# Kernel tuning notes

Measured on AMD Instinct MI355X. Metric: run time of the kernel, lower is better.

The kernel has to match this reference:

```python
import jax, jax.numpy as jnp
import numpy as np

B, T, D_IN, H, L, OUT, S = 128, 256, 8, 512, 2, 2, 32
A = H  # attention_size == hidden_size


def lstm_cell(h, c, xt, Wih, Whh, b):
    # PyTorch LSTM gate order: i, f, g, o ; b = b_ih + b_hh (combined)
    g = xt @ Wih.T + h @ Whh.T + b
    i, f, gg, o = jnp.split(g, 4, axis=-1)
    c = jax.nn.sigmoid(f) * c + jax.nn.sigmoid(i) * jnp.tanh(gg)
    h = jax.nn.sigmoid(o) * jnp.tanh(c)
    return h, c


def setup_inputs() -> dict:
    key = jax.random.key(0)
    ks = jax.random.split(key, 20)
    w = lambda k, shape: jax.random.normal(k, shape, jnp.float32) * 0.1
    return {
        "x": jax.random.normal(ks[0], (B, T, D_IN), jnp.float32),
        # bidirectional encoder, 2 layers; leading dim 2 = (fwd, bwd)
        "enc_Wih0": w(ks[1], (2, 4 * H, D_IN)),
        "enc_Whh0": w(ks[2], (2, 4 * H, H)),
        "enc_b0": w(ks[3], (2, 4 * H)),
        "enc_Wih1": w(ks[4], (2, 4 * H, 2 * H)),
        "enc_Whh1": w(ks[5], (2, 4 * H, H)),
        "enc_b1": w(ks[6], (2, 4 * H)),
        # unidirectional decoder, 2 layers; layer0 input = output_size + 2H
        "dec_Wih0": w(ks[7], (4 * H, 2 * H + OUT)),
        "dec_Whh0": w(ks[8], (4 * H, H)),
        "dec_b0": w(ks[9], (4 * H,)),
        "dec_Wih1": w(ks[10], (4 * H, H)),
        "dec_Whh1": w(ks[11], (4 * H, H)),
        "dec_b1": w(ks[12], (4 * H,)),
        # Bahdanau attention (no biases)
        "Wa": w(ks[13], (A, 2 * H)),
        "Ua": w(ks[14], (A, H)),
        "Va": w(ks[15], (1, A)),
        "proj_W": w(ks[16], (H, H)),
        "proj_b": jnp.zeros((H,), jnp.float32),
        "fc_W": w(ks[17], (OUT, H)),
        "fc_b": jnp.zeros((OUT,), jnp.float32),
    }


def _forward(x, enc_Wih0, enc_Whh0, enc_b0, enc_Wih1, enc_Whh1, enc_b1,
             dec_Wih0, dec_Whh0, dec_b0, dec_Wih1, dec_Whh1, dec_b1,
             Wa, Ua, Va, proj_W, proj_b, fc_W, fc_b):
    Bb = x.shape[0]
    xT = jnp.swapaxes(x, 0, 1)  # [T,B,D]

    def run_dir(seq, Wih, Whh, b, reverse):
        h0 = jnp.zeros((Bb, H), x.dtype)
        def step(carry, xt):
            h, c = lstm_cell(carry[0], carry[1], xt, Wih, Whh, b)
            return (h, c), h
        (hT, cT), hs = jax.lax.scan(step, (h0, h0), seq, reverse=reverse)
        return hs, hT, cT

    # encoder layer 0 (bidirectional)
    of, hf0, cf0 = run_dir(xT, enc_Wih0[0], enc_Whh0[0], enc_b0[0], False)
    ob, hb0, cb0 = run_dir(xT, enc_Wih0[1], enc_Whh0[1], enc_b0[1], True)
    l1in = jnp.concatenate([of, ob], -1)  # [T,B,2H]
    # encoder layer 1
    of1, hf1, cf1 = run_dir(l1in, enc_Wih1[0], enc_Whh1[0], enc_b1[0], False)
    ob1, hb1, cb1 = run_dir(l1in, enc_Wih1[1], enc_Whh1[1], enc_b1[1], True)
    enc_out = jnp.swapaxes(jnp.concatenate([of1, ob1], -1), 0, 1)  # [B,T,2H]

    # torch hidden order: [l0_fwd, l0_bwd, l1_fwd, l1_bwd]; code takes first num_layers=2
    dh = jnp.tanh(jnp.stack([hf0, hb0]) @ proj_W.T + proj_b)  # [2,B,H]
    dc = jnp.stack([cf0, cb0])

    Wa_vals = enc_out @ Wa.T  # [B,T,A], loop-invariant part of attention
    y0 = x[:, -1, :OUT]

    def dec_step(carry, _):
        h, c, y = carry
        q = h[-1]  # [B,H] last-layer hidden
        score = jnp.tanh(Wa_vals + (q @ Ua.T)[:, None, :]) @ Va.T  # [B,T,1]
        wts = jax.nn.softmax(score, axis=1)
        z = jnp.sum(wts * enc_out, axis=1)  # [B,2H]
        h0n, c0n = lstm_cell(h[0], c[0], jnp.concatenate([y, z], 1), dec_Wih0, dec_Whh0, dec_b0)
        h1n, c1n = lstm_cell(h[1], c[1], h0n, dec_Wih1, dec_Whh1, dec_b1)
        yn = h1n @ fc_W.T + fc_b  # [B,OUT]
        return (jnp.stack([h0n, h1n]), jnp.stack([c0n, c1n]), yn), yn

    _, ys = jax.lax.scan(dec_step, (dh, dc, y0), None, length=S)
    return jnp.swapaxes(ys, 0, 1)  # [B,S,OUT]


def reference(x, enc_Wih0, enc_Whh0, enc_b0, enc_Wih1, enc_Whh1, enc_b1,
              dec_Wih0, dec_Whh0, dec_b0, dec_Wih1, dec_Whh1, dec_b1,
              Wa, Ua, Va, proj_W, proj_b, fc_W, fc_b):
    return _forward(x, enc_Wih0, enc_Whh0, enc_b0, enc_Wih1, enc_Whh1, enc_b1,
                    dec_Wih0, dec_Whh0, dec_b0, dec_Wih1, dec_Whh1, dec_b1,
                    Wa, Ua, Va, proj_W, proj_b, fc_W, fc_b)
```

## Files before the change

### kernel.cpp

```cpp
#include <hip/hip_runtime.h>

typedef _Float16 h16;
typedef __attribute__((ext_vector_type(8))) _Float16 f16x8;
typedef __attribute__((ext_vector_type(4))) float f32x4;
typedef unsigned long long u64;
typedef unsigned int u32;
typedef unsigned short u16;

#define B_ 128
#define T_ 256
#define H_ 512
#define S_ 32
#define MFMA __builtin_amdgcn_mfma_f32_16x16x32_f16

#define SLOT_L0F 0
#define SLOT_L0B 257
#define SLOT_ALL 514
#define SLOT_L1F 515
#define SLOT_L1B 771
#define SLOT_DEC 1027

__device__ __forceinline__ float fexp2(float x){ return __builtin_amdgcn_exp2f(x); }
__device__ __forceinline__ float frcp (float x){ return __builtin_amdgcn_rcpf(x); }
__device__ __forceinline__ float fsig (float x){ return frcp(1.f + fexp2(-1.44269504089f*x)); }
__device__ __forceinline__ float ftanh(float x){ return 1.f - 2.f*frcp(1.f + fexp2(2.88539008178f*x)); }

__device__ __forceinline__ f16x8 ld16_coh(const h16* p) {
  u64 q0 = __hip_atomic_load((const u64*)p,     __ATOMIC_RELAXED, __HIP_MEMORY_SCOPE_AGENT);
  u64 q1 = __hip_atomic_load((const u64*)p + 1, __ATOMIC_RELAXED, __HIP_MEMORY_SCOPE_AGENT);
  u64 a[2] = {q0, q1};
  f16x8 v; __builtin_memcpy(&v, a, 16);
  return v;
}
__device__ __forceinline__ float ld4f_coh(const float* p) {
  u32 b = __hip_atomic_load((const u32*)p, __ATOMIC_RELAXED, __HIP_MEMORY_SCOPE_AGENT);
  float v; __builtin_memcpy(&v, &b, 4);
  return v;
}
__device__ __forceinline__ float ld2h_coh(const h16* p) {
  u16 b = __hip_atomic_load((const u16*)p, __ATOMIC_RELAXED, __HIP_MEMORY_SCOPE_AGENT);
  h16 v; __builtin_memcpy(&v, &b, 2);
  return (float)v;
}
__device__ __forceinline__ void st2_coh(h16* p, h16 v) {
  u16 b; __builtin_memcpy(&b, &v, 2);
  __hip_atomic_store((u16*)p, b, __ATOMIC_RELAXED, __HIP_MEMORY_SCOPE_AGENT);
}
__device__ __forceinline__ void st4_coh(float* p, float v) {
  u32 b; __builtin_memcpy(&b, &v, 4);
  __hip_atomic_store((u32*)p, b, __ATOMIC_RELAXED, __HIP_MEMORY_SCOPE_AGENT);
}

__device__ __forceinline__ void bar_arrive(u32* c, int tid) {
  __syncthreads();
  if (tid == 0) atomicAdd(c, 1u);
}
__device__ __forceinline__ void bar_wait(const u32* c, u32 n) {
  while (__hip_atomic_load(c, __ATOMIC_RELAXED, __HIP_MEMORY_SCOPE_AGENT) < n) {}
  __builtin_amdgcn_sched_barrier(0);
}

struct EncP {
  const h16 *xpad, *Wih0, *Whh0, *Wih1, *Whh1;
  const float *b0, *b1;
  h16 *l1in, *encout;
  float *cdump;
  u32* cnt;
};

__global__ __launch_bounds__(512, 1) void encoder_persist(EncP P) {
  const int wg = blockIdx.x, dir = wg >> 7;
  const int j0 = (wg & 127) << 2;
  const int tid = threadIdx.x, wid = tid >> 6, lane = tid & 63;
  const int col = lane & 15, rowg = lane >> 4;
  const int u = col & 3, gt = col >> 2;
  const int m0 = wid << 4;

  __shared__ h16 W[16][1544];

  auto stage = [&](const h16* Wih, int Kx, const h16* Whh) {
    const int CX = Kx >> 3, CT = CX + 64;
    for (int i = tid; i < 16 * CT; i += 512) {
      const int r = i / CT, c = i - r * CT;
      const int grow = (r >> 2) * 512 + j0 + (r & 3);
      f16x8 v = (c < CX) ? *(const f16x8*)(Wih + (size_t)grow * Kx + (c << 3))
                         : *(const f16x8*)(Whh + (size_t)grow * 512 + ((c - CX) << 3));
      *(f16x8*)(&W[r][c << 3]) = v;
    }
  };
  auto pick = [&](float own, float p4, float p8, float p12, int x) {
    return x == 0 ? own : x == 1 ? p4 : x == 2 ? p8 : p12;
  };
  auto xpart0 = [&](int t) -> f32x4 {
    f32x4 a = {0.f, 0.f, 0.f, 0.f};
    f16x8 av = *(const f16x8*)(P.xpad + ((size_t)(m0 + col) * T_ + t) * 32 + rowg * 8);
    f16x8 bv = *(const f16x8*)(&W[col][rowg * 8]);
    return MFMA(av, bv, a, 0, 0, 0);
  };
  auto xpart1 = [&](int t) -> f32x4 {
    f32x4 a = {0.f, 0.f, 0.f, 0.f};
    const h16* ax = P.l1in + ((size_t)t * B_ + m0 + col) * 1024 + rowg * 8;
    #pragma unroll
    for (int ks = 0; ks < 32; ++ks) {
      f16x8 av = *(const f16x8*)(ax + ks * 32);
      f16x8 bv = *(const f16x8*)(&W[col][ks * 32 + rowg * 8]);
      a = MFMA(av, bv, a, 0, 0, 0);
    }
    return a;
  };

  u32* cL0 = P.cnt + (size_t)(dir ? SLOT_L0B : SLOT_L0F) * 16;
  u32* cL1 = P.cnt + (size_t)(dir ? SLOT_L1B : SLOT_L1F) * 16;
  u32* cAll = P.cnt + (size_t)SLOT_ALL * 16;

  float c0_ = 0.f, c1_ = 0.f, c2_ = 0.f, c3_ = 0.f;
  float h0, h1, h2, h3;

#define GATECOMB(av_, cvar, hvar, bias_)                                        \
  { float a_ = av_ + bias_;                                                     \
    float p4_ = __shfl_xor(a_, 4), p8_ = __shfl_xor(a_, 8), p12_ = __shfl_xor(a_, 12); \
    float iv = pick(a_, p4_, p8_, p12_, gt);                                    \
    float fv = pick(a_, p4_, p8_, p12_, gt ^ 1);                                \
    float gv = pick(a_, p4_, p8_, p12_, gt ^ 2);                                \
    float ov = pick(a_, p4_, p8_, p12_, gt ^ 3);                                \
    cvar = fsig(fv) * cvar + fsig(iv) * ftanh(gv);                              \
    hvar = fsig(ov) * ftanh(cvar); }

  stage(P.Wih0 + (size_t)dir * 2048 * 32, 32, P.Whh0 + (size_t)dir * 2048 * 512);
  const float bias0 = P.b0[dir * 2048 + gt * 512 + j0 + u];
  __syncthreads();

  f32x4 accx = xpart0(dir ? 255 : 0);
  for (int i = 0; i < 256; ++i) {
    const int t = dir ? 255 - i : i;
    f32x4 acc = accx;
    if (i) {
      bar_wait(cL0 + (size_t)(i - 1) * 16, 128);
      const int tp = dir ? t + 1 : t - 1;
      const h16* ah = P.l1in + ((size_t)tp * B_ + m0 + col) * 1024 + dir * 512 + rowg * 8;
      #pragma unroll
      for (int ks = 0; ks < 16; ++ks) {
        f16x8 av = ld16_coh(ah + ks * 32);
        f16x8 bv = *(const f16x8*)(&W[col][32 + ks * 32 + rowg * 8]);
        acc = MFMA(av, bv, acc, 0, 0, 0);
      }
    }
    GATECOMB(acc[0], c0_, h0, bias0) GATECOMB(acc[1], c1_, h1, bias0)
    GATECOMB(acc[2], c2_, h2, bias0) GATECOMB(acc[3], c3_, h3, bias0)
    const float hw = (gt == 0) ? h0 : (gt == 1) ? h1 : (gt == 2) ? h2 : h3;
    const int bm = m0 + (rowg << 2) + gt;
    st2_coh(&P.l1in[((size_t)t * B_ + bm) * 1024 + dir * 512 + j0 + u], (h16)hw);
    bar_arrive(cL0 + (size_t)i * 16, tid);
    if (i < 255) accx = xpart0(dir ? 254 - i : i + 1);
  }
  {
    const float cw = (gt == 0) ? c0_ : (gt == 1) ? c1_ : (gt == 2) ? c2_ : c3_;
    const int bm = m0 + (rowg << 2) + gt;
    P.cdump[(size_t)dir * B_ * H_ + (size_t)bm * H_ + j0 + u] = cw;
  }
  bar_arrive(cAll, tid);
  bar_wait(cAll, 256);

  stage(P.Wih1 + (size_t)dir * 2048 * 1024, 1024, P.Whh1 + (size_t)dir * 2048 * 512);
  const float bias1 = P.b1[dir * 2048 + gt * 512 + j0 + u];
  c0_ = c1_ = c2_ = c3_ = 0.f;
  __syncthreads();

  accx = xpart1(dir ? 255 : 0);
  for (int i = 0; i < 256; ++i) {
    const int t = dir ? 255 - i : i;
    f32x4 acc = accx;
    if (i) {
      bar_wait(cL1 + (size_t)(i - 1) * 16, 128);
      const int tp = dir ? t + 1 : t - 1;
      const h16* ah = P.encout + ((size_t)(m0 + col) * T_ + tp) * 1024 + dir * 512 + rowg * 8;
      #pragma unroll
      for (int ks = 0; ks < 16; ++ks) {
        f16x8 av = ld16_coh(ah + ks * 32);
        f16x8 bv = *(const f16x8*)(&W[col][1024 + ks * 32 + rowg * 8]);
        acc = MFMA(av, bv, acc, 0, 0, 0);
      }
    }
    GATECOMB(acc[0], c0_, h0, bias1) GATECOMB(acc[1], c1_, h1, bias1)
    GATECOMB(acc[2], c2_, h2, bias1) GATECOMB(acc[3], c3_, h3, bias1)
    const float hw = (gt == 0) ? h0 : (gt == 1) ? h1 : (gt == 2) ? h2 : h3;
    const int bm = m0 + (rowg << 2) + gt;
    st2_coh(&P.encout[((size_t)bm * T_ + t) * 1024 + dir * 512 + j0 + u], (h16)hw);
    bar_arrive(cL1 + (size_t)i * 16, tid);
    if (i < 255) accx = xpart1(dir ? 254 - i : i + 1);
  }
#undef GATECOMB
}

struct DecP {
  const h16 *bUa, *WaV, *enc, *bdWih0, *bdWhh0, *bdWih1, *bdWhh1;
  const float *Va, *db0, *db1, *fcW, *fcb, *cdump;
  float *qUa, *score, *out;
  h16 *xcat, *dh0, *dh1;
  u32* cnt;
};

__global__ __launch_bounds__(512, 1) void decoder_persist(DecP D) {
  const int wg = blockIdx.x, tid = threadIdx.x;
  const int wid = tid >> 6, lane = tid & 63;
  const int col = lane & 15, rowg = lane >> 4;
  const int gw = wg * 8 + wid;
  const int mt = wg >> 5, ut = wg & 31;
  const int mi = tid >> 4, ji = tid & 15;

  __shared__ h16 Ast[16][1576];
  __shared__ float gtl[4][16][16];
  __shared__ float sred[256], swts[256];

  u32* cD = D.cnt + (size_t)SLOT_DEC * 16;
  u32 ep = 0;
  auto dbar = [&]() {
    bar_arrive(cD + (size_t)ep * 16, tid);
    bar_wait(cD + (size_t)ep * 16, 256);
    ++ep;
  };

  float c0r = 0.f, c1r = 0.f;
  if (tid < 256) {
    c0r = D.cdump[(size_t)(mt * 16 + mi) * 512 + ut * 16 + ji];
    c1r = D.cdump[(size_t)B_ * H_ + (size_t)(mt * 16 + mi) * 512 + ut * 16 + ji];
  }

  for (int s = 0; s < S_; ++s) {
    const int par = s & 1;
    const h16* h1c = D.dh1 + (size_t)par * B_ * H_;
    h16* h1n = D.dh1 + (size_t)(par ^ 1) * B_ * H_;
    const h16* h0c = D.dh0 + (size_t)par * B_ * H_;
    h16* h0n = D.dh0 + (size_t)(par ^ 1) * B_ * H_;

    if (gw < 256) {
      const int qmt = gw >> 5, qnt = gw & 31;
      f32x4 acc = {0, 0, 0, 0};
      const h16* ap = h1c + (size_t)(qmt * 16 + col) * 512 + rowg * 8;
      const h16* bp = D.bUa + (size_t)(qnt * 16 + col) * 512 + rowg * 8;
      #pragma unroll
      for (int kc = 0; kc < 16; ++kc) {
        f16x8 av = ld16_coh(ap + kc * 32);
        f16x8 bv = *(const f16x8*)(bp + kc * 32);
        acc = MFMA(av, bv, acc, 0, 0, 0);
      }
      #pragma unroll
      for (int t2 = 0; t2 < 4; ++t2)
        st4_coh(D.qUa + (size_t)(qmt * 16 + rowg * 4 + t2) * 512 + qnt * 16 + col, acc[t2]);
    } else if (gw < 512 && s > 0) {
      const int idx = gw - 256, m = idx >> 1, o = idx & 1;
      float sum = 0.f;
      #pragma unroll
      for (int i2 = 0; i2 < 8; ++i2) {
        const int k = i2 * 64 + lane;
        sum += ld2h_coh(h1c + (size_t)m * 512 + k) * D.fcW[o * 512 + k];
      }
      #pragma unroll
      for (int o2 = 32; o2; o2 >>= 1) sum += __shfl_xor(sum, o2);
      if (lane == 0) {
        const float y = sum + D.fcb[o];
        D.out[(size_t)m * (S_ * 2) + (s - 1) * 2 + o] = y;
        st2_coh(D.xcat + (size_t)m * 1056 + o, (h16)y);
      }
    }
    dbar();

    {
      const int m = gw >> 4, tg = gw & 15;
      float q[8], va[8];
      #pragma unroll
      for (int i2 = 0; i2 < 8; ++i2) {
        q[i2] = ld4f_coh(D.qUa + (size_t)m * 512 + i2 * 64 + lane);
        va[i2] = D.Va[i2 * 64 + lane];
      }
      for (int tt = 0; tt < 16; ++tt) {
        const int t = tg * 16 + tt;
        const h16* wrow = D.WaV + ((size_t)m * 256 + t) * 512;
        float ssum = 0.f;
        #pragma unroll
        for (int i2 = 0; i2 < 8; ++i2)
          ssum += ftanh((float)wrow[i2 * 64 + lane] + q[i2]) * va[i2];
        #pragma unroll
        for (int o2 = 32; o2; o2 >>= 1) ssum += __shfl_xor(ssum, o2);
        if (lane == 0) st4_coh(D.score + (size_t)m * 256 + t, ssum);
      }
    }
    dbar();

    if (wg < 128) {
      const int m = wg;
      const float sv = (tid < 256) ? ld4f_coh(D.score + (size_t)m * 256 + tid) : -1e30f;
      if (tid < 256) sred[tid] = sv;
      __syncthreads();
      for (int o2 = 128; o2; o2 >>= 1) { if (tid < o2) sred[tid] = fmaxf(sred[tid], sred[tid + o2]); __syncthreads(); }
      const float mx = sred[0]; __syncthreads();
      const float p = (tid < 256) ? fexp2((sv - mx) * 1.44269504089f) : 0.f;
      if (tid < 256) sred[tid] = p;
      __syncthreads();
      for (int o2 = 128; o2; o2 >>= 1) { if (tid < o2) sred[tid] += sred[tid + o2]; __syncthreads(); }
      if (tid < 256) swts[tid] = p * frcp(sred[0]);
      __syncthreads();
      const h16* erow = D.enc + (size_t)m * 256 * 1024;
      #pragma unroll
      for (int half = 0; half < 2; ++half) {
        const int k = tid + half * 512;
        float a0 = 0, a1 = 0, a2 = 0, a3 = 0;
        for (int t = 0; t < 256; t += 4) {
          a0 += swts[t    ] * (float)erow[(t    ) * 1024 + k];
          a1 += swts[t + 1] * (float)erow[(t + 1) * 1024 + k];
          a2 += swts[t + 2] * (float)erow[(t + 2) * 1024 + k];
          a3 += swts[t + 3] * (float)erow[(t + 3) * 1024 + k];
        }
        st2_coh(D.xcat + (size_t)m * 1056 + 2 + k, (h16)((a0 + a1) + (a2 + a3)));
      }
    }
    dbar();

    {
      for (int i2 = tid; i2 < 16 * 196; i2 += 512) {
        const int r = i2 / 196, c = i2 - r * 196;
        f16x8 v = (c < 132) ? ld16_coh(D.xcat + (size_t)(mt * 16 + r) * 1056 + c * 8)
                            : ld16_coh(h0c + (size_t)(mt * 16 + r) * 512 + (c - 132) * 8);
        *(f16x8*)&Ast[r][c * 8] = v;
      }
      __syncthreads();
      if (wid < 4) {
        const int n = wid * 512 + ut * 16 + col;
        f32x4 acc = {0, 0, 0, 0};
        const h16* w1 = D.bdWih0 + (size_t)n * 1056 + rowg * 8;
        const h16* w2 = D.bdWhh0 + (size_t)n * 512 + rowg * 8;
        #pragma unroll
        for (int kc = 0; kc < 33; ++kc) {
          f16x8 av = *(const f16x8*)&Ast[col][kc * 32 + rowg * 8];
          f16x8 bv = *(const f16x8*)(w1 + kc * 32);
          acc = MFMA(av, bv, acc, 0, 0, 0);
        }
        #pragma unroll
        for (int kc = 0; kc < 16; ++kc) {
          f16x8 av = *(const f16x8*)&Ast[col][1056 + kc * 32 + rowg * 8];
          f16x8 bv = *(const f16x8*)(w2 + kc * 32);
          acc = MFMA(av, bv, acc, 0, 0, 0);
        }
        #pragma unroll
        for (int t2 = 0; t2 < 4; ++t2) gtl[wid][rowg * 4 + t2][col] = acc[t2];
      }
      __syncthreads();
      if (tid < 256) {
        const int jj = ut * 16 + ji;
        const float iv = gtl[0][mi][ji] + D.db0[jj];
        const float fv = gtl[1][mi][ji] + D.db0[512 + jj];
        const float gv = gtl[2][mi][ji] + D.db0[1024 + jj];
        const float ov = gtl[3][mi][ji] + D.db0[1536 + jj];
        c0r = fsig(fv) * c0r + fsig(iv) * ftanh(gv);
        st2_coh(h0n + (size_t)(mt * 16 + mi) * 512 + jj, (h16)(fsig(ov) * ftanh(c0r)));
      }
    }
    dbar();

    {
      for (int i2 = tid; i2 < 16 * 128; i2 += 512) {
        const int r = i2 >> 7, c = i2 & 127;
        f16x8 v = (c < 64) ? ld16_coh(h0n + (size_t)(mt * 16 + r) * 512 + c * 8)
                           : ld16_coh(h1c + (size_t)(mt * 16 + r) * 512 + (c - 64) * 8);
        *(f16x8*)&Ast[r][c * 8] = v;
      }
      __syncthreads();
      if (wid < 4) {
        const int n = wid * 512 + ut * 16 + col;
        f32x4 acc = {0, 0, 0, 0};
        const h16* w1 = D.bdWih1 + (size_t)n * 512 + rowg * 8;
        const h16* w2 = D.bdWhh1 + (size_t)n * 512 + rowg * 8;
        #pragma unroll
        for (int kc = 0; kc < 16; ++kc) {
          f16x8 av = *(const f16x8*)&Ast[col][kc * 32 + rowg * 8];
          f16x8 bv = *(const f16x8*)(w1 + kc * 32);
          acc = MFMA(av, bv, acc, 0, 0, 0);
        }
        #pragma unroll
        for (int kc = 0; kc < 16; ++kc) {
          f16x8 av = *(const f16x8*)&Ast[col][512 + kc * 32 + rowg * 8];
          f16x8 bv = *(const f16x8*)(w2 + kc * 32);
          acc = MFMA(av, bv, acc, 0, 0, 0);
        }
        #pragma unroll
        for (int t2 = 0; t2 < 4; ++t2) gtl[wid][rowg * 4 + t2][col] = acc[t2];
      }
      __syncthreads();
      if (tid < 256) {
        const int jj = ut * 16 + ji;
        const float iv = gtl[0][mi][ji] + D.db1[jj];
        const float fv = gtl[1][mi][ji] + D.db1[512 + jj];
        const float gv = gtl[2][mi][ji] + D.db1[1024 + jj];
        const float ov = gtl[3][mi][ji] + D.db1[1536 + jj];
        c1r = fsig(fv) * c1r + fsig(iv) * ftanh(gv);
        st2_coh(h1n + (size_t)(mt * 16 + mi) * 512 + jj, (h16)(fsig(ov) * ftanh(c1r)));
      }
    }
    dbar();
  }

  if (gw < 256) {
    const int m = gw >> 1, o = gw & 1;
    const h16* h1f = D.dh1;
    float sum = 0.f;
    #pragma unroll
    for (int i2 = 0; i2 < 8; ++i2) {
      const int k = i2 * 64 + lane;
      sum += ld2h_coh(h1f + (size_t)m * 512 + k) * D.fcW[o * 512 + k];
    }
    #pragma unroll
    for (int o2 = 32; o2; o2 >>= 1) sum += __shfl_xor(sum, o2);
    if (lane == 0) D.out[(size_t)m * (S_ * 2) + (S_ - 1) * 2 + o] = sum + D.fcb[o];
  }
}

__global__ __launch_bounds__(256) void gemm_tn(const h16* Am, int lda, const h16* Bm,
                                               const float* bias, void* Cout, int ldc,
                                               int K, int mode) {
  const int wid = threadIdx.x >> 6, lane = threadIdx.x & 63;
  const int r = lane & 15, g = lane >> 4;
  const int m0 = (blockIdx.x * 4 + wid) * 16;
  const int n0 = blockIdx.y * 64;
  f32x4 acc[4] = {{0,0,0,0},{0,0,0,0},{0,0,0,0},{0,0,0,0}};
  const h16* ap = Am + (size_t)(m0 + r) * lda + g * 8;
  const h16* bp = Bm + (size_t)(n0 + r) * K + g * 8;
  for (int k = 0; k < K; k += 32) {
    f16x8 av = *(const f16x8*)(ap + k);
    #pragma unroll
    for (int j = 0; j < 4; ++j) {
      f16x8 bv = *(const f16x8*)(bp + (size_t)j * 16 * K + k);
      acc[j] = MFMA(av, bv, acc[j], 0, 0, 0);
    }
  }
  #pragma unroll
  for (int j = 0; j < 4; ++j) {
    const int n = n0 + j * 16 + r;
    const float badd = bias ? bias[n] : 0.f;
    #pragma unroll
    for (int t = 0; t < 4; ++t) {
      const int m = m0 + g * 4 + t;
      float v = acc[j][t] + badd;
      if (mode == 2) v = ftanh(v);
      if (mode == 0) ((float*)Cout)[(size_t)m * ldc + n] = v;
      else           ((h16*)Cout) [(size_t)m * ldc + n] = (h16)v;
    }
  }
}

__global__ void convert_pad(const float* __restrict__ in, h16* __restrict__ out,
                            int rows, int Kin, int Kout) {
  const size_t i = (size_t)blockIdx.x * 256 + threadIdx.x;
  if (i >= (size_t)rows * Kout) return;
  const int r = (int)(i / Kout), k = (int)(i % Kout);
  out[i] = (k < Kin) ? (h16)in[(size_t)r * Kin + k] : (h16)0.f;
}

__global__ void y0_init(const float* __restrict__ x, h16* __restrict__ xcat) {
  const int tid = threadIdx.x;
  if (tid < 256) {
    const int m = tid >> 1, o = tid & 1;
    xcat[(size_t)m * 1056 + o] = (h16)x[(size_t)(m * T_ + (T_ - 1)) * 8 + o];
  }
}

extern "C" void kernel_launch(void* const* d_in, const int* in_sizes, int n_in,
                              void* d_out, int out_size, void* d_ws, size_t ws_size,
                              hipStream_t stream) {
  const float* x     = (const float*)d_in[0];
  const float* eWih0 = (const float*)d_in[1];
  const float* eWhh0 = (const float*)d_in[2];
  const float* eb0   = (const float*)d_in[3];
  const float* eWih1 = (const float*)d_in[4];
  const float* eWhh1 = (const float*)d_in[5];
  const float* eb1   = (const float*)d_in[6];
  const float* dWih0 = (const float*)d_in[7];
  const float* dWhh0 = (const float*)d_in[8];
  const float* db0   = (const float*)d_in[9];
  const float* dWih1 = (const float*)d_in[10];
  const float* dWhh1 = (const float*)d_in[11];
  const float* db1   = (const float*)d_in[12];
  const float* Wa    = (const float*)d_in[13];
  const float* Ua    = (const float*)d_in[14];
  const float* Va    = (const float*)d_in[15];
  const float* projW = (const float*)d_in[16];
  const float* projb = (const float*)d_in[17];
  const float* fcW   = (const float*)d_in[18];
  const float* fcb   = (const float*)d_in[19];
  float* out = (float*)d_out;

  size_t cur = 0;
  auto alloc = [&](size_t bytes) {
    void* p = (char*)d_ws + cur;
    cur += (bytes + 255) & ~(size_t)255;
    return p;
  };
  h16*  xpad   = (h16*) alloc((size_t)B_ * T_ * 32 * 2);
  h16*  l1in   = (h16*) alloc((size_t)T_ * B_ * 1024 * 2);
  h16*  encout = (h16*) alloc((size_t)B_ * T_ * 1024 * 2);
  h16*  WaV    = (h16*) alloc((size_t)B_ * T_ * H_ * 2);
  float* cdump = (float*)alloc((size_t)2 * B_ * H_ * 4);
  float* score = (float*)alloc((size_t)B_ * T_ * 4);
  float* qUa   = (float*)alloc((size_t)B_ * H_ * 4);
  h16*  xcat   = (h16*) alloc((size_t)B_ * 1056 * 2);
  h16*  dh0    = (h16*) alloc((size_t)2 * B_ * H_ * 2);
  h16*  dh1    = (h16*) alloc((size_t)2 * B_ * H_ * 2);
  u32*  cnt    = (u32*) alloc((size_t)2048 * 16 * 4);
  h16*  bWih0  = (h16*) alloc((size_t)2 * 2048 * 32 * 2);
  h16*  bWhh0  = (h16*) alloc((size_t)2 * 2048 * 512 * 2);
  h16*  bWih1  = (h16*) alloc((size_t)2 * 2048 * 1024 * 2);
  h16*  bWhh1  = (h16*) alloc((size_t)2 * 2048 * 512 * 2);
  h16*  bdWih0 = (h16*) alloc((size_t)2048 * 1056 * 2);
  h16*  bdWhh0 = (h16*) alloc((size_t)2048 * 512 * 2);
  h16*  bdWih1 = (h16*) alloc((size_t)2048 * 512 * 2);
  h16*  bdWhh1 = (h16*) alloc((size_t)2048 * 512 * 2);
  h16*  bWa    = (h16*) alloc((size_t)512 * 1024 * 2);
  h16*  bUa    = (h16*) alloc((size_t)512 * 512 * 2);
  h16*  bprojW = (h16*) alloc((size_t)512 * 512 * 2);
  if (cur > ws_size) return;

  (void)hipMemsetAsync(cnt, 0, (size_t)2048 * 16 * 4, stream);
  (void)hipMemsetAsync(xcat, 0, (size_t)B_ * 1056 * 2, stream);

  auto conv = [&](const float* in, h16* o, int rows, int kin, int kout) {
    const size_t total = (size_t)rows * kout;
    convert_pad<<<dim3((unsigned)((total + 255) / 256)), dim3(256), 0, stream>>>(in, o, rows, kin, kout);
  };
  conv(x,     xpad,   B_ * T_,  8,    32);
  conv(eWih0, bWih0,  2 * 2048, 8,    32);
  conv(eWhh0, bWhh0,  2 * 2048, 512,  512);
  conv(eWih1, bWih1,  2 * 2048, 1024, 1024);
  conv(eWhh1, bWhh1,  2 * 2048, 512,  512);
  conv(dWih0, bdWih0, 2048,     1026, 1056);
  conv(dWhh0, bdWhh0, 2048,     512,  512);
  conv(dWih1, bdWih1, 2048,     512,  512);
  conv(dWhh1, bdWhh1, 2048,     512,  512);
  conv(Wa,    bWa,    512,      1024, 1024);
  conv(Ua,    bUa,    512,      512,  512);
  conv(projW, bprojW, 512,      512,  512);

  EncP P;
  P.xpad = xpad; P.Wih0 = bWih0; P.Whh0 = bWhh0; P.Wih1 = bWih1; P.Whh1 = bWhh1;
  P.b0 = eb0; P.b1 = eb1; P.l1in = l1in; P.encout = encout; P.cdump = cdump; P.cnt = cnt;
  encoder_persist<<<dim3(256), dim3(512), 0, stream>>>(P);

  gemm_tn<<<dim3(B_ * T_ / 64, 8), dim3(256), 0, stream>>>(encout, 1024, bWa, nullptr, WaV, 512, 1024, 1);
  gemm_tn<<<dim3(B_ / 64, 8), dim3(256), 0, stream>>>(l1in + (size_t)(T_ - 1) * B_ * 1024, 1024,
                                                      bprojW, projb, dh0, 512, 512, 2);
  gemm_tn<<<dim3(B_ / 64, 8), dim3(256), 0, stream>>>(l1in + 512, 1024,
                                                      bprojW, projb, dh1, 512, 512, 2);
  y0_init<<<dim3(1), dim3(256), 0, stream>>>(x, xcat);

  DecP D;
  D.bUa = bUa; D.WaV = WaV; D.enc = encout;
  D.bdWih0 = bdWih0; D.bdWhh0 = bdWhh0; D.bdWih1 = bdWih1; D.bdWhh1 = bdWhh1;
  D.Va = Va; D.db0 = db0; D.db1 = db1; D.fcW = fcW; D.fcb = fcb; D.cdump = cdump;
  D.qUa = qUa; D.score = score; D.out = out;
  D.xcat = xcat; D.dh0 = dh0; D.dh1 = dh1;
  D.cnt = cnt;
  decoder_persist<<<dim3(256), dim3(512), 0, stream>>>(D);
}
```

Baseline: 12.43 ms.

## Halve encoder workgroups and spread grid barrier counters over multiple cache lines

The encoder now runs 128 workgroups, each computing 8 hidden units per direction with two accumulator tiles, so fewer groups take part in each per-timestep grid barrier. Barrier counters are split across 8 cache lines per epoch, and one wavefront polls all lines with s_sleep backoff followed by a __syncthreads. This is meant to cut atomic contention and polling traffic on single counters, in both the encoder and the decoder barriers. The trade-off is twice the per-workgroup MFMA work and LDS (32 rows) on a sequential critical path, with half as many CUs in use.

```diff
diff --git a/kernel.cpp b/kernel.cpp
--- a/kernel.cpp
+++ b/kernel.cpp
@@ -13,12 +13,9 @@
 #define S_ 32
 #define MFMA __builtin_amdgcn_mfma_f32_16x16x32_f16
 
-#define SLOT_L0F 0
-#define SLOT_L0B 257
-#define SLOT_ALL 514
-#define SLOT_L1F 515
-#define SLOT_L1B 771
-#define SLOT_DEC 1027
+#define ALL_BASE 8192
+#define DEC_BASE 8200
+#define N_LINES  (8192 + 8 + 1280)
 
 __device__ __forceinline__ float fexp2(float x){ return __builtin_amdgcn_exp2f(x); }
 __device__ __forceinline__ float frcp (float x){ return __builtin_amdgcn_rcpf(x); }
@@ -51,12 +48,22 @@
   __hip_atomic_store((u32*)p, b, __ATOMIC_RELAXED, __HIP_MEMORY_SCOPE_AGENT);
 }
 
-__device__ __forceinline__ void bar_arrive(u32* c, int tid) {
+__device__ __forceinline__ void bar_arrive(u32* cnt, int base, int line, int tid) {
   __syncthreads();
-  if (tid == 0) atomicAdd(c, 1u);
-}
-__device__ __forceinline__ void bar_wait(const u32* c, u32 n) {
-  while (__hip_atomic_load(c, __ATOMIC_RELAXED, __HIP_MEMORY_SCOPE_AGENT) < n) {}
+  if (tid == 0) atomicAdd(cnt + (size_t)(base + line) * 16, 1u);
+}
+__device__ __forceinline__ void bar_wait(const u32* cnt, int base, u32 per_line,
+                                         int tid, int lane) {
+  if (tid < 64) {
+    for (;;) {
+      u32 v = (lane < 8) ? __hip_atomic_load(cnt + (size_t)(base + lane) * 16,
+                                             __ATOMIC_RELAXED, __HIP_MEMORY_SCOPE_AGENT)
+                         : per_line;
+      if (__all(v >= per_line)) break;
+      __builtin_amdgcn_s_sleep(8);
+    }
+  }
+  __syncthreads();
   __builtin_amdgcn_sched_barrier(0);
 }
 
@@ -69,20 +76,22 @@
 };
 
 __global__ __launch_bounds__(512, 1) void encoder_persist(EncP P) {
-  const int wg = blockIdx.x, dir = wg >> 7;
-  const int j0 = (wg & 127) << 2;
+  const int wg = blockIdx.x, dir = wg >> 6;
+  const int j0 = (wg & 63) << 3;
+  const int lineid = wg & 7;
   const int tid = threadIdx.x, wid = tid >> 6, lane = tid & 63;
   const int col = lane & 15, rowg = lane >> 4;
   const int u = col & 3, gt = col >> 2;
   const int m0 = wid << 4;
 
-  __shared__ h16 W[16][1544];
+  __shared__ h16 W[32][1544];
 
   auto stage = [&](const h16* Wih, int Kx, const h16* Whh) {
     const int CX = Kx >> 3, CT = CX + 64;
-    for (int i = tid; i < 16 * CT; i += 512) {
+    for (int i = tid; i < 32 * CT; i += 512) {
       const int r = i / CT, c = i - r * CT;
-      const int grow = (r >> 2) * 512 + j0 + (r & 3);
+      const int rr = r & 15;
+      const int grow = (rr >> 2) * 512 + j0 + ((r >> 4) << 2) + (rr & 3);
       f16x8 v = (c < CX) ? *(const f16x8*)(Wih + (size_t)grow * Kx + (c << 3))
                          : *(const f16x8*)(Whh + (size_t)grow * 512 + ((c - CX) << 3));
       *(f16x8*)(&W[r][c << 3]) = v;
@@ -91,30 +100,13 @@
   auto pick = [&](float own, float p4, float p8, float p12, int x) {
     return x == 0 ? own : x == 1 ? p4 : x == 2 ? p8 : p12;
   };
-  auto xpart0 = [&](int t) -> f32x4 {
-    f32x4 a = {0.f, 0.f, 0.f, 0.f};
-    f16x8 av = *(const f16x8*)(P.xpad + ((size_t)(m0 + col) * T_ + t) * 32 + rowg * 8);
-    f16x8 bv = *(const f16x8*)(&W[col][rowg * 8]);
-    return MFMA(av, bv, a, 0, 0, 0);
-  };
-  auto xpart1 = [&](int t) -> f32x4 {
-    f32x4 a = {0.f, 0.f, 0.f, 0.f};
-    const h16* ax = P.l1in + ((size_t)t * B_ + m0 + col) * 1024 + rowg * 8;
-    #pragma unroll
-    for (int ks = 0; ks < 32; ++ks) {
-      f16x8 av = *(const f16x8*)(ax + ks * 32);
-      f16x8 bv = *(const f16x8*)(&W[col][ks * 32 + rowg * 8]);
-      a = MFMA(av, bv, a, 0, 0, 0);
-    }
-    return a;
-  };
-
-  u32* cL0 = P.cnt + (size_t)(dir ? SLOT_L0B : SLOT_L0F) * 16;
-  u32* cL1 = P.cnt + (size_t)(dir ? SLOT_L1B : SLOT_L1F) * 16;
-  u32* cAll = P.cnt + (size_t)SLOT_ALL * 16;
-
-  float c0_ = 0.f, c1_ = 0.f, c2_ = 0.f, c3_ = 0.f;
-  float h0, h1, h2, h3;
+
+  const int base_l0 = dir * 2048;
+  const int base_l1 = 4096 + dir * 2048;
+
+  float cA0 = 0.f, cA1 = 0.f, cA2 = 0.f, cA3 = 0.f;
+  float cB0 = 0.f, cB1 = 0.f, cB2 = 0.f, cB3 = 0.f;
+  float hA0, hA1, hA2, hA3, hB0, hB1, hB2, hB3;
 
 #define GATECOMB(av_, cvar, hvar, bias_)                                        \
   { float a_ = av_ + bias_;                                                     \
@@ -127,67 +119,105 @@
     hvar = fsig(ov) * ftanh(cvar); }
 
   stage(P.Wih0 + (size_t)dir * 2048 * 32, 32, P.Whh0 + (size_t)dir * 2048 * 512);
-  const float bias0 = P.b0[dir * 2048 + gt * 512 + j0 + u];
+  const float bA0 = P.b0[dir * 2048 + gt * 512 + j0 + u];
+  const float bB0 = P.b0[dir * 2048 + gt * 512 + j0 + 4 + u];
   __syncthreads();
 
-  f32x4 accx = xpart0(dir ? 255 : 0);
+  f32x4 accA, accB;
+  {
+    const int t0 = dir ? 255 : 0;
+    f16x8 av = *(const f16x8*)(P.xpad + ((size_t)(m0 + col) * T_ + t0) * 32 + rowg * 8);
+    f32x4 z = {0.f, 0.f, 0.f, 0.f};
+    accA = MFMA(av, *(const f16x8*)(&W[col][rowg * 8]), z, 0, 0, 0);
+    accB = MFMA(av, *(const f16x8*)(&W[16 + col][rowg * 8]), z, 0, 0, 0);
+  }
   for (int i = 0; i < 256; ++i) {
     const int t = dir ? 255 - i : i;
-    f32x4 acc = accx;
     if (i) {
-      bar_wait(cL0 + (size_t)(i - 1) * 16, 128);
+      bar_wait(P.cnt, base_l0 + (i - 1) * 8, 8, tid, lane);
       const int tp = dir ? t + 1 : t - 1;
       const h16* ah = P.l1in + ((size_t)tp * B_ + m0 + col) * 1024 + dir * 512 + rowg * 8;
       #pragma unroll
       for (int ks = 0; ks < 16; ++ks) {
         f16x8 av = ld16_coh(ah + ks * 32);
-        f16x8 bv = *(const f16x8*)(&W[col][32 + ks * 32 + rowg * 8]);
-        acc = MFMA(av, bv, acc, 0, 0, 0);
-      }
-    }
-    GATECOMB(acc[0], c0_, h0, bias0) GATECOMB(acc[1], c1_, h1, bias0)
-    GATECOMB(acc[2], c2_, h2, bias0) GATECOMB(acc[3], c3_, h3, bias0)
-    const float hw = (gt == 0) ? h0 : (gt == 1) ? h1 : (gt == 2) ? h2 : h3;
+        accA = MFMA(av, *(const f16x8*)(&W[col][32 + ks * 32 + rowg * 8]), accA, 0, 0, 0);
+        accB = MFMA(av, *(const f16x8*)(&W[16 + col][32 + ks * 32 + rowg * 8]), accB, 0, 0, 0);
+      }
+    }
+    GATECOMB(accA[0], cA0, hA0, bA0) GATECOMB(accA[1], cA1, hA1, bA0)
+    GATECOMB(accA[2], cA2, hA2, bA0) GATECOMB(accA[3], cA3, hA3, bA0)
+    GATECOMB(accB[0], cB0, hB0, bB0) GATECOMB(accB[1], cB1, hB1, bB0)
+    GATECOMB(accB[2], cB2, hB2, bB0) GATECOMB(accB[3], cB3, hB3, bB0)
+    const float hwA = (gt == 0) ? hA0 : (gt == 1) ? hA1 : (gt == 2) ? hA2 : hA3;
+    const float hwB = (gt == 0) ? hB0 : (gt == 1) ? hB1 : (gt == 2) ? hB2 : hB3;
     const int bm = m0 + (rowg << 2) + gt;
-    st2_coh(&P.l1in[((size_t)t * B_ + bm) * 1024 + dir * 512 + j0 + u], (h16)hw);
-    bar_arrive(cL0 + (size_t)i * 16, tid);
-    if (i < 255) accx = xpart0(dir ? 254 - i : i + 1);
+    h16* hp = &P.l1in[((size_t)t * B_ + bm) * 1024 + dir * 512 + j0 + u];
+    st2_coh(hp, (h16)hwA);
+    st2_coh(hp + 4, (h16)hwB);
+    bar_arrive(P.cnt, base_l0 + i * 8, lineid, tid);
+    if (i < 255) {
+      const int tn = dir ? 254 - i : i + 1;
+      f16x8 av = *(const f16x8*)(P.xpad + ((size_t)(m0 + col) * T_ + tn) * 32 + rowg * 8);
+      f32x4 z = {0.f, 0.f, 0.f, 0.f};
+      accA = MFMA(av, *(const f16x8*)(&W[col][rowg * 8]), z, 0, 0, 0);
+      accB = MFMA(av, *(const f16x8*)(&W[16 + col][rowg * 8]), z, 0, 0, 0);
+    }
   }
   {
-    const float cw = (gt == 0) ? c0_ : (gt == 1) ? c1_ : (gt == 2) ? c2_ : c3_;
+    const float cwA = (gt == 0) ? cA0 : (gt == 1) ? cA1 : (gt == 2) ? cA2 : cA3;
+    const float cwB = (gt == 0) ? cB0 : (gt == 1) ? cB1 : (gt == 2) ? cB2 : cB3;
     const int bm = m0 + (rowg << 2) + gt;
-    P.cdump[(size_t)dir * B_ * H_ + (size_t)bm * H_ + j0 + u] = cw;
-  }
-  bar_arrive(cAll, tid);
-  bar_wait(cAll, 256);
+    float* cp = &P.cdump[(size_t)dir * B_ * H_ + (size_t)bm * H_ + j0 + u];
+    cp[0] = cwA;
+    cp[4] = cwB;
+  }
+  bar_arrive(P.cnt, ALL_BASE, lineid, tid);
+  bar_wait(P.cnt, ALL_BASE, 16, tid, lane);
 
   stage(P.Wih1 + (size_t)dir * 2048 * 1024, 1024, P.Whh1 + (size_t)dir * 2048 * 512);
-  const float bias1 = P.b1[dir * 2048 + gt * 512 + j0 + u];
-  c0_ = c1_ = c2_ = c3_ = 0.f;
+  const float bA1 = P.b1[dir * 2048 + gt * 512 + j0 + u];
+  const float bB1 = P.b1[dir * 2048 + gt * 512 + j0 + 4 + u];
+  cA0 = cA1 = cA2 = cA3 = cB0 = cB1 = cB2 = cB3 = 0.f;
   __syncthreads();
 
-  accx = xpart1(dir ? 255 : 0);
+  auto xpart1 = [&](int t, f32x4& a, f32x4& b) {
+    f32x4 z = {0.f, 0.f, 0.f, 0.f};
+    a = z; b = z;
+    const h16* ax = P.l1in + ((size_t)t * B_ + m0 + col) * 1024 + rowg * 8;
+    #pragma unroll
+    for (int ks = 0; ks < 32; ++ks) {
+      f16x8 av = *(const f16x8*)(ax + ks * 32);
+      a = MFMA(av, *(const f16x8*)(&W[col][ks * 32 + rowg * 8]), a, 0, 0, 0);
+      b = MFMA(av, *(const f16x8*)(&W[16 + col][ks * 32 + rowg * 8]), b, 0, 0, 0);
+    }
+  };
+
+  xpart1(dir ? 255 : 0, accA, accB);
   for (int i = 0; i < 256; ++i) {
     const int t = dir ? 255 - i : i;
-    f32x4 acc = accx;
     if (i) {
-      bar_wait(cL1 + (size_t)(i - 1) * 16, 128);
+      bar_wait(P.cnt, base_l1 + (i - 1) * 8, 8, tid, lane);
       const int tp = dir ? t + 1 : t - 1;
       const h16* ah = P.encout + ((size_t)(m0 + col) * T_ + tp) * 1024 + dir * 512 + rowg * 8;
       #pragma unroll
       for (int ks = 0; ks < 16; ++ks) {
         f16x8 av = ld16_coh(ah + ks * 32);
-        f16x8 bv = *(const f16x8*)(&W[col][1024 + ks * 32 + rowg * 8]);
-        acc = MFMA(av, bv, acc, 0, 0, 0);
-      }
-    }
-    GATECOMB(acc[0], c0_, h0, bias1) GATECOMB(acc[1], c1_, h1, bias1)
-    GATECOMB(acc[2], c2_, h2, bias1) GATECOMB(acc[3], c3_, h3, bias1)
-    const float hw = (gt == 0) ? h0 : (gt == 1) ? h1 : (gt == 2) ? h2 : h3;
+        accA = MFMA(av, *(const f16x8*)(&W[col][1024 + ks * 32 + rowg * 8]), accA, 0, 0, 0);
+        accB = MFMA(av, *(const f16x8*)(&W[16 + col][1024 + ks * 32 + rowg * 8]), accB, 0, 0, 0);
+      }
+    }
+    GATECOMB(accA[0], cA0, hA0, bA1) GATECOMB(accA[1], cA1, hA1, bA1)
+    GATECOMB(accA[2], cA2, hA2, bA1) GATECOMB(accA[3], cA3, hA3, bA1)
+    GATECOMB(accB[0], cB0, hB0, bB1) GATECOMB(accB[1], cB1, hB1, bB1)
+    GATECOMB(accB[2], cB2, hB2, bB1) GATECOMB(accB[3], cB3, hB3, bB1)
+    const float hwA = (gt == 0) ? hA0 : (gt == 1) ? hA1 : (gt == 2) ? hA2 : hA3;
+    const float hwB = (gt == 0) ? hB0 : (gt == 1) ? hB1 : (gt == 2) ? hB2 : hB3;
     const int bm = m0 + (rowg << 2) + gt;
-    st2_coh(&P.encout[((size_t)bm * T_ + t) * 1024 + dir * 512 + j0 + u], (h16)hw);
-    bar_arrive(cL1 + (size_t)i * 16, tid);
-    if (i < 255) accx = xpart1(dir ? 254 - i : i + 1);
+    h16* hp = &P.encout[((size_t)bm * T_ + t) * 1024 + dir * 512 + j0 + u];
+    st2_coh(hp, (h16)hwA);
+    st2_coh(hp + 4, (h16)hwB);
+    bar_arrive(P.cnt, base_l1 + i * 8, lineid, tid);
+    if (i < 255) xpart1(dir ? 254 - i : i + 1, accA, accB);
   }
 #undef GATECOMB
 }
@@ -207,16 +237,16 @@
   const int gw = wg * 8 + wid;
   const int mt = wg >> 5, ut = wg & 31;
   const int mi = tid >> 4, ji = tid & 15;
+  const int lineid = wg & 7;
 
   __shared__ h16 Ast[16][1576];
   __shared__ float gtl[4][16][16];
   __shared__ float sred[256], swts[256];
 
-  u32* cD = D.cnt + (size_t)SLOT_DEC * 16;
-  u32 ep = 0;
+  int ep = 0;
   auto dbar = [&]() {
-    bar_arrive(cD + (size_t)ep * 16, tid);
-    bar_wait(cD + (size_t)ep * 16, 256);
+    bar_arrive(D.cnt, DEC_BASE + ep * 8, lineid, tid);
+    bar_wait(D.cnt, DEC_BASE + ep * 8, 32, tid, lane);
     ++ep;
   };
 
@@ -332,14 +362,12 @@
         #pragma unroll
         for (int kc = 0; kc < 33; ++kc) {
           f16x8 av = *(const f16x8*)&Ast[col][kc * 32 + rowg * 8];
-          f16x8 bv = *(const f16x8*)(w1 + kc * 32);
-          acc = MFMA(av, bv, acc, 0, 0, 0);
+          acc = MFMA(av, *(const f16x8*)(w1 + kc * 32), acc, 0, 0, 0);
         }
         #pragma unroll
         for (int kc = 0; kc < 16; ++kc) {
           f16x8 av = *(const f16x8*)&Ast[col][1056 + kc * 32 + rowg * 8];
-          f16x8 bv = *(const f16x8*)(w2 + kc * 32);
-          acc = MFMA(av, bv, acc, 0, 0, 0);
+          acc = MFMA(av, *(const f16x8*)(w2 + kc * 32), acc, 0, 0, 0);
         }
         #pragma unroll
         for (int t2 = 0; t2 < 4; ++t2) gtl[wid][rowg * 4 + t2][col] = acc[t2];
@@ -373,14 +401,12 @@
         #pragma unroll
         for (int kc = 0; kc < 16; ++kc) {
           f16x8 av = *(const f16x8*)&Ast[col][kc * 32 + rowg * 8];
-          f16x8 bv = *(const f16x8*)(w1 + kc * 32);
-          acc = MFMA(av, bv, acc, 0, 0, 0);
+          acc = MFMA(av, *(const f16x8*)(w1 + kc * 32), acc, 0, 0, 0);
         }
         #pragma unroll
         for (int kc = 0; kc < 16; ++kc) {
           f16x8 av = *(const f16x8*)&Ast[col][512 + kc * 32 + rowg * 8];
-          f16x8 bv = *(const f16x8*)(w2 + kc * 32);
-          acc = MFMA(av, bv, acc, 0, 0, 0);
+          acc = MFMA(av, *(const f16x8*)(w2 + kc * 32), acc, 0, 0, 0);
         }
         #pragma unroll
         for (int t2 = 0; t2 < 4; ++t2) gtl[wid][rowg * 4 + t2][col] = acc[t2];
@@ -504,7 +530,7 @@
   h16*  xcat   = (h16*) alloc((size_t)B_ * 1056 * 2);
   h16*  dh0    = (h16*) alloc((size_t)2 * B_ * H_ * 2);
   h16*  dh1    = (h16*) alloc((size_t)2 * B_ * H_ * 2);
-  u32*  cnt    = (u32*) alloc((size_t)2048 * 16 * 4);
+  u32*  cnt    = (u32*) alloc((size_t)N_LINES * 64);
   h16*  bWih0  = (h16*) alloc((size_t)2 * 2048 * 32 * 2);
   h16*  bWhh0  = (h16*) alloc((size_t)2 * 2048 * 512 * 2);
   h16*  bWih1  = (h16*) alloc((size_t)2 * 2048 * 1024 * 2);
@@ -518,7 +544,7 @@
   h16*  bprojW = (h16*) alloc((size_t)512 * 512 * 2);
   if (cur > ws_size) return;
 
-  (void)hipMemsetAsync(cnt, 0, (size_t)2048 * 16 * 4, stream);
+  (void)hipMemsetAsync(cnt, 0, (size_t)N_LINES * 64, stream);
   (void)hipMemsetAsync(xcat, 0, (size_t)B_ * 1056 * 2, stream);
 
   auto conv = [&](const float* in, h16* o, int rows, int kin, int kout) {
@@ -541,7 +567,7 @@
   EncP P;
   P.xpad = xpad; P.Wih0 = bWih0; P.Whh0 = bWhh0; P.Wih1 = bWih1; P.Whh1 = bWhh1;
   P.b0 = eb0; P.b1 = eb1; P.l1in = l1in; P.encout = encout; P.cdump = cdump; P.cnt = cnt;
-  encoder_persist<<<dim3(256), dim3(512), 0, stream>>>(P);
+  encoder_persist<<<dim3(128), dim3(512), 0, stream>>>(P);
 
   gemm_tn<<<dim3(B_ * T_ / 64, 8), dim3(256), 0, stream>>>(encout, 1024, bWa, nullptr, WaV, 512, 1024, 1);
   gemm_tn<<<dim3(B_ / 64, 8), dim3(256), 0, stream>>>(l1in + (size_t)(T_ - 1) * B_ * 1024, 1024,
```

After: 10.86 ms. 12.6% less time.
